# Kernel tuning notes

Measured on AMD Instinct MI355X. Metric: run time of the kernel, lower is better.

The kernel has to match this reference:

```python
import jax, jax.numpy as jnp
import numpy as np
from jax import lax

C = 256   # cnn_channels == rnn_in_dim
H = 256   # rnn_out_dim
NB = 16   # nb_classes
B, T, F = 16, 512, 40


def setup_inputs() -> dict:
    key = jax.random.key(0)
    ks = jax.random.split(key, 16)
    d = {
        'x': jax.random.normal(ks[0], (B, T, F), jnp.float32),
        'w1': jax.random.normal(ks[1], (C, 1, 5, 5), jnp.float32) * 0.05,
        'b1': jax.random.normal(ks[2], (C,), jnp.float32) * 0.05,
        'g1': jax.random.uniform(ks[3], (C,), jnp.float32, 0.5, 1.5),
        'bt1': jax.random.normal(ks[4], (C,), jnp.float32) * 0.05,
        'm1': jnp.zeros((C,), jnp.float32),
        'v1': jnp.ones((C,), jnp.float32),
        'w2': jax.random.normal(ks[5], (C, C, 5, 5), jnp.float32) * 0.02,
        'b2': jax.random.normal(ks[6], (C,), jnp.float32) * 0.05,
        'g2': jax.random.uniform(ks[7], (C,), jnp.float32, 0.5, 1.5),
        'bt2': jax.random.normal(ks[8], (C,), jnp.float32) * 0.05,
        'm2': jnp.zeros((C,), jnp.float32),
        'v2': jnp.ones((C,), jnp.float32),
        'w3': jax.random.normal(ks[9], (C, C, 5, 5), jnp.float32) * 0.02,
        'b3': jax.random.normal(ks[10], (C,), jnp.float32) * 0.05,
        'g3': jax.random.uniform(ks[11], (C,), jnp.float32, 0.5, 1.5),
        'bt3': jax.random.normal(ks[12], (C,), jnp.float32) * 0.05,
        'm3': jnp.zeros((C,), jnp.float32),
        'v3': jnp.ones((C,), jnp.float32),
        'w_ih': jax.random.normal(ks[13], (3 * H, C), jnp.float32) * 0.05,
        'w_hh': jax.random.normal(ks[14], (3 * H, H), jnp.float32) * 0.05,
        'b_ih': jnp.zeros((3 * H,), jnp.float32),
        'b_hh': jnp.zeros((3 * H,), jnp.float32),
        'w_cls': jax.random.normal(ks[15], (NB, H), jnp.float32) * 0.05,
        'b_cls': jnp.zeros((NB,), jnp.float32),
    }
    return d


def _conv_block(x, w, b, g, bt, m, v, pool):
    # Conv2d(k=5, pad=2) + BN (eval mode) + ReLU + MaxPool over freq axis
    y = lax.conv_general_dilated(x, w, (1, 1), ((2, 2), (2, 2)),
                                 dimension_numbers=('NCHW', 'OIHW', 'NCHW'))
    y = y + b[None, :, None, None]
    y = (y - m[None, :, None, None]) * (g * lax.rsqrt(v + 1e-5))[None, :, None, None] + bt[None, :, None, None]
    y = jnp.maximum(y, 0.0)
    y = lax.reduce_window(y, -jnp.inf, lax.max, (1, 1, 1, pool), (1, 1, 1, pool), 'VALID')
    return y


def _crnn(x, w1, b1, g1, bt1, m1, v1, w2, b2, g2, bt2, m2, v2,
          w3, b3, g3, bt3, m3, v3, w_ih, w_hh, b_ih, b_hh, w_cls, b_cls):
    b_size, t_steps, _ = x.shape
    y = x[:, None, :, :]                              # [B,1,T,F]
    y = _conv_block(y, w1, b1, g1, bt1, m1, v1, 5)    # [B,C,T,8]
    y = _conv_block(y, w2, b2, g2, bt2, m2, v2, 4)    # [B,C,T,2]
    y = _conv_block(y, w3, b3, g3, bt3, m3, v3, 2)    # [B,C,T,1]
    feats = jnp.transpose(y, (0, 2, 1, 3)).reshape(b_size, t_steps, C)  # [B,T,C]

    # Precompute input-side GRU gates for all steps (math identical to per-step)
    gi_all = jnp.einsum('btc,gc->btg', feats, w_ih) + b_ih  # [B,T,3H]

    def step(h, gi_t):
        gh = h @ w_hh.T + b_hh                        # [B,3H]
        r = jax.nn.sigmoid(gi_t[:, :H] + gh[:, :H])
        z = jax.nn.sigmoid(gi_t[:, H:2 * H] + gh[:, H:2 * H])
        n = jnp.tanh(gi_t[:, 2 * H:] + r * gh[:, 2 * H:])
        h_new = (1.0 - z) * n + z * h
        out = h_new @ w_cls.T + b_cls                 # [B,NB]
        return h_new, out

    h0 = jnp.zeros((b_size, H), feats.dtype)
    _, outs = lax.scan(step, h0, jnp.swapaxes(gi_all, 0, 1))  # [T,B,NB]
    return jnp.swapaxes(outs, 0, 1)                   # [B,T,NB]


def reference(x, w1, b1, g1, bt1, m1, v1, w2, b2, g2, bt2, m2, v2,
              w3, b3, g3, bt3, m3, v3, w_ih, w_hh, b_ih, b_hh, w_cls, b_cls):
    return _crnn(x, w1, b1, g1, bt1, m1, v1, w2, b2, g2, bt2, m2, v2,
                 w3, b3, g3, bt3, m3, v3, w_ih, w_hh, b_ih, b_hh, w_cls, b_cls)
```

## Files before the change

kernel.cpp:

```cpp
#include <hip/hip_runtime.h>
#include <hip/hip_bf16.h>
#include <math.h>

#define BB 16
#define TT 512
#define FF 40
#define CC 256
#define HH 256
#define GG 768
#define NB 16

typedef _Float16 f16;
typedef __attribute__((ext_vector_type(8))) _Float16 f16x8;
typedef __attribute__((ext_vector_type(4))) _Float16 f16x4;
typedef __attribute__((ext_vector_type(4))) float f32x4;

#define O_OUT1 0u
#define O_GI   0u
#define O_OUT2 16777216u
#define O_OUT3 20971520u
#define O_W2P  23068672u
#define O_W3P  24707072u
#define O_WIHP 26345472u
#define O_WHHP 26443776u

__device__ __forceinline__ float sigm_fast(float x) {
    return __builtin_amdgcn_rcpf(1.f + __expf(-x));
}
__device__ __forceinline__ float tanh_fast(float x) {
    return 1.f - 2.f * __builtin_amdgcn_rcpf(1.f + __expf(2.f * x));
}

__device__ __forceinline__ float sel4(f32x4 v, int q1, int q2) {
    float lo = q1 ? v[1] : v[0];
    float hi = q1 ? v[3] : v[2];
    return q2 ? hi : lo;
}

__device__ __forceinline__ void pack768(const float* __restrict__ src, f16* __restrict__ dst, int e) {
    int lane = e & 63;
    int r1 = e >> 6;
    int tile = r1 % 48, kf = r1 / 48;
    int g = tile * 16 + (lane & 15);
    int k0 = kf * 32 + (lane >> 4) * 8;
    f16x8 v;
#pragma unroll
    for (int j = 0; j < 8; ++j)
        v[j] = (f16)src[(size_t)g * HH + k0 + j];
    *(f16x8*)(dst + (size_t)e * 8) = v;
}

__global__ __launch_bounds__(256) void pack_all_kernel(
    const float* __restrict__ w2, const float* __restrict__ w3,
    const float* __restrict__ wih, const float* __restrict__ whh,
    const float* __restrict__ wcls,
    f16* __restrict__ w2p, f16* __restrict__ w3p, f16* __restrict__ wihp,
    f16* __restrict__ whhp, f16* __restrict__ wclsp) {
    int blk = blockIdx.x;
    int tid = threadIdx.x;
    if (blk < 800) {
        int e = blk * 256 + tid;
        int lane = e & 63;
        int r1 = e >> 6;
        int ntile = r1 & 15;
        int r2 = r1 >> 4;
        int cs4 = r2 & 3;
        int r3 = r2 >> 2;
        int cs = r3 & 1;
        int tap = r3 >> 1;
        int co = ntile * 16 + (lane & 15);
        int ci0 = cs * 128 + cs4 * 32 + (lane >> 4) * 8;
        f16x8 v;
#pragma unroll
        for (int j = 0; j < 8; ++j)
            v[j] = (f16)w2[(size_t)co * 6400 + (ci0 + j) * 25 + tap];
        *(f16x8*)(w2p + (size_t)e * 8) = v;
    } else if (blk < 1280) {
        int e = (blk - 800) * 256 + tid;
        int lane = e & 63;
        int r1 = e >> 6;
        int ntile = r1 & 15;
        int r2 = r1 >> 4;
        int cs4 = r2 & 3;
        int r3 = r2 >> 2;
        int cs = r3 & 1;
        int tap = r3 >> 1;
        int kh = tap / 3, kw = tap % 3 + 1;
        int co = ntile * 16 + (lane & 15);
        int ci0 = cs * 128 + cs4 * 32 + (lane >> 4) * 8;
        f16x8 v;
#pragma unroll
        for (int j = 0; j < 8; ++j)
            v[j] = (f16)w3[(size_t)co * 6400 + (ci0 + j) * 25 + kh * 5 + kw];
        *(f16x8*)(w3p + (size_t)e * 8) = v;
    } else if (blk < 1376) {
        pack768(wih, wihp, (blk - 1280) * 256 + tid);
    } else if (blk < 1472) {
        pack768(whh, whhp, (blk - 1376) * 256 + tid);
    } else {
#pragma unroll
        for (int i = 0; i < 2; ++i) {
            int e = tid + i * 256;
            int lane = e & 63, kf = e >> 6;
            int nb = lane & 15;
            int c0 = kf * 32 + (lane >> 4) * 8;
            f16x8 v;
#pragma unroll
            for (int j = 0; j < 8; ++j)
                v[j] = (f16)wcls[nb * HH + c0 + j];
            *(f16x8*)(wclsp + (size_t)e * 8) = v;
        }
    }
}

__global__ __launch_bounds__(256) void conv1_kernel(
    const float* __restrict__ x, const float* __restrict__ w1,
    const float* __restrict__ b1, const float* __restrict__ g1,
    const float* __restrict__ bt1, const float* __restrict__ m1,
    const float* __restrict__ v1, f16* __restrict__ out1h) {
    int h = blockIdx.x;
    int b = blockIdx.y;
    int c = threadIdx.x;
    __shared__ float xs[5][44];
    int t = threadIdx.x;
    if (t < 220) {
        int rr = t / 44, cc = t % 44;
        int hh = h + rr - 2, ww = cc - 2;
        float v = 0.f;
        if (hh >= 0 && hh < TT && ww >= 0 && ww < FF) v = x[(b * TT + hh) * FF + ww];
        xs[rr][cc] = v;
    }
    __syncthreads();
    float wr[25];
#pragma unroll
    for (int i = 0; i < 25; ++i) wr[i] = w1[c * 25 + i];
    float sc = g1[c] * rsqrtf(v1[c] + 1e-5f);
    float sh = (b1[c] - m1[c]) * sc + bt1[c];
    float conv[40];
#pragma unroll
    for (int w = 0; w < 40; ++w) conv[w] = 0.f;
#pragma unroll
    for (int kh = 0; kh < 5; ++kh) {
        float rr[44];
#pragma unroll
        for (int i = 0; i < 44; ++i) rr[i] = xs[kh][i];
#pragma unroll
        for (int kw = 0; kw < 5; ++kw) {
            float wv = wr[kh * 5 + kw];
#pragma unroll
            for (int w = 0; w < 40; ++w) conv[w] += rr[w + kw] * wv;
        }
    }
    f16* op = out1h + ((size_t)(b * TT + h) * 8) * CC + c;
#pragma unroll
    for (int j = 0; j < 8; ++j) {
        float m = 0.f;
#pragma unroll
        for (int p = 0; p < 5; ++p) m = fmaxf(m, conv[j * 5 + p] * sc + sh);
        op[j * CC] = (f16)m;
    }
}

__global__ __launch_bounds__(256) void conv2_mfma_kernel(
    const f16* __restrict__ in, const f16* __restrict__ w2p,
    const float* __restrict__ b2, const float* __restrict__ g2,
    const float* __restrict__ bt2, const float* __restrict__ m2,
    const float* __restrict__ v2, f16* __restrict__ out2h) {
    int htile = blockIdx.x;
    int b = blockIdx.y;
    int h0 = htile * 8;
    int t = threadIdx.x;
    int lane = t & 63, wid = t >> 6;
    int m16 = lane & 15, kq = lane >> 4;

    __shared__ f16 lds_a[12 * 12 * 136];

#pragma unroll
    for (int i = 0; i < 39; ++i) {
        int idx = t + i * 256;
        if (idx < 9792) ((unsigned*)lds_a)[idx] = 0u;
    }
    __syncthreads();

    f32x4 acc[4][4];
#pragma unroll
    for (int mf = 0; mf < 4; ++mf)
#pragma unroll
        for (int nf = 0; nf < 4; ++nf) acc[mf][nf] = (f32x4)(0.f);

    for (int cs = 0; cs < 2; ++cs) {
        if (cs) __syncthreads();
#pragma unroll
        for (int i = 0; i < 6; ++i) {
            int q = t + i * 256;
            int row = q >> 7, rem = q & 127;
            int w = rem >> 4, ci8 = (rem & 15) * 8;
            int hp = h0 - 2 + row;
            f16x8 v = (f16x8)((f16)0.f);
            if (hp >= 0 && hp < TT)
                v = *(const f16x8*)&in[((size_t)(b * TT + hp) * 8 + w) * CC + cs * 128 + ci8];
            *(f16x8*)&lds_a[row * 1632 + (w + 2) * 136 + ci8] = v;
        }
        __syncthreads();
        for (int kh = 0; kh < 5; ++kh) {
#pragma unroll
            for (int kw = 0; kw < 5; ++kw) {
                int tap = kh * 5 + kw;
#pragma unroll
                for (int cs4 = 0; cs4 < 4; ++cs4) {
                    f16x8 af[4];
#pragma unroll
                    for (int mf = 0; mf < 4; ++mf) {
                        int m = mf * 16 + m16;
                        int row = (m >> 3) + kh;
                        int wp = (m & 7) + kw;
                        af[mf] = *(const f16x8*)&lds_a[row * 1632 + wp * 136 + cs4 * 32 + kq * 8];
                    }
                    const f16x8* bp = (const f16x8*)w2p
                        + ((size_t)(((tap * 2 + cs) * 4 + cs4) * 16 + wid * 4) * 64 + lane);
#pragma unroll
                    for (int nf = 0; nf < 4; ++nf) {
                        f16x8 bf = bp[nf * 64];
#pragma unroll
                        for (int mf = 0; mf < 4; ++mf)
                            acc[mf][nf] = __builtin_amdgcn_mfma_f32_16x16x32_f16(af[mf], bf, acc[mf][nf], 0, 0, 0);
                    }
                }
            }
        }
    }

#pragma unroll
    for (int nf = 0; nf < 4; ++nf) {
        int co = wid * 64 + nf * 16 + m16;
        float sc = g2[co] * rsqrtf(v2[co] + 1e-5f);
        float sh = (b2[co] - m2[co]) * sc + bt2[co];
#pragma unroll
        for (int mf = 0; mf < 4; ++mf) {
            f32x4 v = acc[mf][nf];
            float p = 0.f;
            p = fmaxf(p, v[0] * sc + sh);
            p = fmaxf(p, v[1] * sc + sh);
            p = fmaxf(p, v[2] * sc + sh);
            p = fmaxf(p, v[3] * sc + sh);
            int dh = mf * 2 + (kq >> 1);
            int wout = kq & 1;
            out2h[((size_t)(b * TT + h0 + dh) * 2 + wout) * CC + co] = (f16)p;
        }
    }
}

__global__ __launch_bounds__(256) void conv3gi_kernel(
    const f16* __restrict__ in, const f16* __restrict__ w3p,
    const float* __restrict__ b3, const float* __restrict__ g3,
    const float* __restrict__ bt3, const float* __restrict__ m3,
    const float* __restrict__ v3, const f16* __restrict__ wihp,
    const float* __restrict__ bih, f16* __restrict__ gi2) {
    int htile = blockIdx.x;
    int b = blockIdx.y;
    int h0 = htile * 16;
    int t = threadIdx.x;
    int lane = t & 63, wid = t >> 6;
    int m16 = lane & 15, quad = lane >> 4;
    int rb = m16 >> 1, wv = m16 & 1;

    __shared__ f16 lds_a[20 * 6 * 136];
    __shared__ f16 feats_s[16 * 264];

    for (int i = t; i < 8160; i += 256) ((unsigned*)lds_a)[i] = 0u;
    __syncthreads();

    f32x4 acc[2][4];
#pragma unroll
    for (int mf = 0; mf < 2; ++mf)
#pragma unroll
        for (int nf = 0; nf < 4; ++nf) acc[mf][nf] = (f32x4)(0.f);

    for (int cs = 0; cs < 2; ++cs) {
        if (cs) __syncthreads();
#pragma unroll
        for (int i = 0; i < 3; ++i) {
            int q = t + i * 256;
            if (q < 640) {
                int row = q >> 5, rem = q & 31;
                int w = rem >> 4, ci8 = (rem & 15) * 8;
                int hp = h0 - 2 + row;
                f16x8 v = (f16x8)((f16)0.f);
                if (hp >= 0 && hp < TT)
                    v = *(const f16x8*)&in[((size_t)(b * TT + hp) * 2 + w) * CC + cs * 128 + ci8];
                *(f16x8*)&lds_a[row * 816 + (w + 2) * 136 + ci8] = v;
            }
        }
        __syncthreads();
        for (int kh = 0; kh < 5; ++kh) {
#pragma unroll
            for (int kw3 = 0; kw3 < 3; ++kw3) {
                int tap = kh * 3 + kw3;
#pragma unroll
                for (int cs4 = 0; cs4 < 4; ++cs4) {
                    f16x8 af[2];
#pragma unroll
                    for (int mf = 0; mf < 2; ++mf) {
                        int row = mf * 8 + rb + kh;
                        int wp = wv + kw3 + 1;
                        af[mf] = *(const f16x8*)&lds_a[row * 816 + wp * 136 + cs4 * 32 + quad * 8];
                    }
                    const f16x8* bp = (const f16x8*)w3p
                        + ((size_t)(((tap * 2 + cs) * 4 + cs4) * 16 + wid * 4) * 64 + lane);
#pragma unroll
                    for (int nf = 0; nf < 4; ++nf) {
                        f16x8 bf = bp[nf * 64];
#pragma unroll
                        for (int mf = 0; mf < 2; ++mf)
                            acc[mf][nf] = __builtin_amdgcn_mfma_f32_16x16x32_f16(af[mf], bf, acc[mf][nf], 0, 0, 0);
                    }
                }
            }
        }
    }

#pragma unroll
    for (int nf = 0; nf < 4; ++nf) {
        int co = wid * 64 + nf * 16 + m16;
        float sc = g3[co] * rsqrtf(v3[co] + 1e-5f);
        float sh = (b3[co] - m3[co]) * sc + bt3[co];
#pragma unroll
        for (int mf = 0; mf < 2; ++mf) {
            f32x4 v = acc[mf][nf];
            float p0 = fmaxf(0.f, fmaxf(v[0], v[1]) * sc + sh);
            p0 = fmaxf(p0, fmaxf(0.f, fminf(v[0], v[1]) * sc + sh));
            float p1 = fmaxf(0.f, fmaxf(v[2], v[3]) * sc + sh);
            p1 = fmaxf(p1, fmaxf(0.f, fminf(v[2], v[3]) * sc + sh));
            int m = mf * 8 + quad * 2;
            feats_s[m * 264 + co] = (f16)p0;
            feats_s[(m + 1) * 264 + co] = (f16)p1;
        }
    }
    __syncthreads();

    f32x4 gacc[12];
#pragma unroll
    for (int i = 0; i < 12; ++i) gacc[i] = (f32x4)(0.f);
#pragma unroll
    for (int kf = 0; kf < 8; ++kf) {
        f16x8 af = *(const f16x8*)&feats_s[m16 * 264 + kf * 32 + quad * 8];
#pragma unroll
        for (int nt = 0; nt < 12; ++nt) {
            f16x8 bf = ((const f16x8*)wihp)[(size_t)(kf * 48 + wid * 12 + nt) * 64 + lane];
            gacc[nt] = __builtin_amdgcn_mfma_f32_16x16x32_f16(af, bf, gacc[nt], 0, 0, 0);
        }
    }
#pragma unroll
    for (int nt = 0; nt < 12; ++nt) {
        int g = (wid * 12 + nt) * 16 + m16;
        float bv = bih[g];
#pragma unroll
        for (int r = 0; r < 4; ++r) {
            int s = h0 + quad * 4 + r;
            gi2[((((size_t)(b >> 2) * TT + s) * GG + g) << 2) + (b & 3)] = (f16)(gacc[nt][r] + bv);
        }
    }
}

__global__ __launch_bounds__(1024) void gru_mfma_kernel(
    const f16* __restrict__ gi2, const f16* __restrict__ whhp,
    const float* __restrict__ bhh, f16* __restrict__ hsave) {
    int blk = blockIdx.x;
    int t = threadIdx.x;
    int w = t >> 6, lane = t & 63;
    int n16 = lane & 15, quad = lane >> 4;
    int r2 = n16 & 3;
    int q1 = quad & 1, q2 = quad >> 1;
    __shared__ f16 hA[2][4 * 272];

    for (int i = t; i < 1088; i += 1024) ((unsigned*)hA)[i] = 0u;

    f16x8 wfrag[8][3];
#pragma unroll
    for (int kf = 0; kf < 8; ++kf)
#pragma unroll
        for (int g = 0; g < 3; ++g)
            wfrag[kf][g] = ((const f16x8*)whhp)[(size_t)(kf * 48 + g * 16 + w) * 64 + lane];
#pragma unroll
    for (int kf = 0; kf < 8; ++kf)
#pragma unroll
        for (int g = 0; g < 3; ++g)
            asm volatile("" : "+v"(wfrag[kf][g]));

    int c = w * 16 + n16;
    float bh0 = bhh[c], bh1 = bhh[HH + c], bh2 = bhh[2 * HH + c];
    float hold = 0.f;
    f16 hprev = (f16)0.f;
    int bg = blk * 4 + quad;

    const f16* gbase = gi2 + (size_t)blk * ((size_t)TT * GG * 4);
    int go0 = c * 4 + quad;
    int go1 = (c + HH) * 4 + quad;
    int go2 = (c + 2 * HH) * 4 + quad;

    f16 gc0 = gbase[go0];
    f16 gc1 = gbase[go1];
    f16 gc2 = gbase[go2];
    const f16* gp = gbase + GG * 4;
    __syncthreads();

    for (int s = 0; s < TT; ++s) {
        const f16* hrow = &hA[s & 1][r2 * 272 + quad * 8];
        f16x8 af[8];
#pragma unroll
        for (int kf = 0; kf < 8; ++kf)
            af[kf] = *(const f16x8*)(hrow + kf * 32);

        f16 gn0 = gp[go0];
        f16 gn1 = gp[go1];
        f16 gn2 = gp[go2];
        gp += GG * 4;
        if (s > 0)
            hsave[((size_t)(s - 1) * 16 + bg) * HH + c] = hprev;

        float x0 = (float)gc0 + bh0;
        float x1 = (float)gc1 + bh1;
        float x2 = (float)gc2;

        f32x4 acc[3];
#pragma unroll
        for (int g = 0; g < 3; ++g) acc[g] = (f32x4)(0.f);
#pragma unroll
        for (int kf = 0; kf < 8; ++kf) {
#pragma unroll
            for (int g = 0; g < 3; ++g)
                acc[g] = __builtin_amdgcn_mfma_f32_16x16x32_f16(af[kf], wfrag[kf][g], acc[g], 0, 0, 0);
        }

        float a0 = sel4(acc[0], q1, q2);
        float a1 = sel4(acc[1], q1, q2);
        float a2 = sel4(acc[2], q1, q2);

        float rr = sigm_fast(x0 + a0);
        float zz = sigm_fast(x1 + a1);
        float nn = tanh_fast(x2 + rr * (bh2 + a2));
        hold = nn + zz * (hold - nn);
        f16 hv = (f16)hold;
        hprev = hv;
        hA[(s + 1) & 1][quad * 272 + c] = hv;
        gc0 = gn0; gc1 = gn1; gc2 = gn2;
        asm volatile("s_waitcnt lgkmcnt(0)\n\ts_barrier" ::: "memory");
    }
    hsave[((size_t)(TT - 1) * 16 + bg) * HH + c] = hprev;
}

__global__ __launch_bounds__(256) void cls_kernel(
    const f16* __restrict__ hsave, const f16* __restrict__ wclsp,
    const float* __restrict__ bcls, float* __restrict__ out) {
    int s = blockIdx.x * 4 + (threadIdx.x >> 6);
    int lane = threadIdx.x & 63;
    int n16 = lane & 15, quad = lane >> 4;
    f32x4 ac = (f32x4)(0.f);
#pragma unroll
    for (int kf = 0; kf < 8; ++kf) {
        f16x8 af = *(const f16x8*)&hsave[((size_t)s * 16 + n16) * 256 + kf * 32 + quad * 8];
        f16x8 bf = ((const f16x8*)wclsp)[kf * 64 + lane];
        ac = __builtin_amdgcn_mfma_f32_16x16x32_f16(af, bf, ac, 0, 0, 0);
    }
    float bc = bcls[n16];
#pragma unroll
    for (int r = 0; r < 4; ++r)
        out[((size_t)(quad * 4 + r) * TT + s) * NB + n16] = ac[r] + bc;
}

extern "C" void kernel_launch(void* const* d_in, const int* in_sizes, int n_in,
                              void* d_out, int out_size, void* d_ws, size_t ws_size,
                              hipStream_t stream) {
    const float* x    = (const float*)d_in[0];
    const float* w1   = (const float*)d_in[1];
    const float* b1   = (const float*)d_in[2];
    const float* g1   = (const float*)d_in[3];
    const float* bt1  = (const float*)d_in[4];
    const float* m1   = (const float*)d_in[5];
    const float* v1   = (const float*)d_in[6];
    const float* w2   = (const float*)d_in[7];
    const float* b2   = (const float*)d_in[8];
    const float* g2   = (const float*)d_in[9];
    const float* bt2  = (const float*)d_in[10];
    const float* m2   = (const float*)d_in[11];
    const float* v2   = (const float*)d_in[12];
    const float* w3   = (const float*)d_in[13];
    const float* b3   = (const float*)d_in[14];
    const float* g3   = (const float*)d_in[15];
    const float* bt3  = (const float*)d_in[16];
    const float* m3   = (const float*)d_in[17];
    const float* v3   = (const float*)d_in[18];
    const float* wih  = (const float*)d_in[19];
    const float* whh  = (const float*)d_in[20];
    const float* bih  = (const float*)d_in[21];
    const float* bhh  = (const float*)d_in[22];
    const float* wcls = (const float*)d_in[23];
    const float* bcls = (const float*)d_in[24];

    float* ws    = (float*)d_ws;
    f16*   out1h = (f16*)(ws + O_OUT1);
    f16*   out2h = (f16*)(ws + O_OUT2);
    f16*   gi2   = (f16*)(ws + O_GI);
    f16*   w2p   = (f16*)(ws + O_W2P);
    f16*   w3p   = (f16*)(ws + O_W3P);
    f16*   wclsp = (f16*)(ws + O_W3P) + 983040;
    f16*   wihp  = (f16*)(ws + O_WIHP);
    f16*   whhp  = (f16*)(ws + O_WHHP);
    f16*   hsave = (f16*)(ws + O_OUT3);
    float* fout  = (float*)d_out;

    pack_all_kernel<<<1473, 256, 0, stream>>>(w2, w3, wih, whh, wcls,
                                              w2p, w3p, wihp, whhp, wclsp);

    conv1_kernel<<<dim3(512, 16), 256, 0, stream>>>(x, w1, b1, g1, bt1, m1, v1, out1h);
    conv2_mfma_kernel<<<dim3(64, 16), 256, 0, stream>>>(out1h, w2p, b2, g2, bt2, m2, v2, out2h);

    conv3gi_kernel<<<dim3(32, 16), 256, 0, stream>>>(out2h, w3p, b3, g3, bt3, m3, v3,
                                                     wihp, bih, gi2);

    gru_mfma_kernel<<<4, 1024, 0, stream>>>(gi2, whhp, bhh, hsave);

    cls_kernel<<<128, 256, 0, stream>>>(hsave, wclsp, bcls, fout);
}
```

Baseline: 1.171 ms.

## Fuse weight packing into conv1 launch and prefetch conv2 second channel half

Merges the weight-packing kernel into the conv1 kernel as extra blocks, removing one launch and letting the packing run alongside conv1. In conv2, the global loads for the second 128-channel half are issued into registers before the first half's MFMA loop, so their latency overlaps that compute, and they are then written to LDS. This raises register pressure in conv2 by six f16x8 values per thread, which may lower occupancy.

```diff
diff --git a/kernel.cpp b/kernel.cpp
--- a/kernel.cpp
+++ b/kernel.cpp
@@ -50,79 +50,82 @@
     *(f16x8*)(dst + (size_t)e * 8) = v;
 }
 
-__global__ __launch_bounds__(256) void pack_all_kernel(
+__global__ __launch_bounds__(256) void conv1_pack_kernel(
+    const float* __restrict__ x, const float* __restrict__ w1,
+    const float* __restrict__ b1, const float* __restrict__ g1,
+    const float* __restrict__ bt1, const float* __restrict__ m1,
+    const float* __restrict__ v1, f16* __restrict__ out1h,
     const float* __restrict__ w2, const float* __restrict__ w3,
     const float* __restrict__ wih, const float* __restrict__ whh,
     const float* __restrict__ wcls,
     f16* __restrict__ w2p, f16* __restrict__ w3p, f16* __restrict__ wihp,
     f16* __restrict__ whhp, f16* __restrict__ wclsp) {
-    int blk = blockIdx.x;
+    __shared__ float xs[5][44];
+    int bid = blockIdx.x;
     int tid = threadIdx.x;
-    if (blk < 800) {
-        int e = blk * 256 + tid;
-        int lane = e & 63;
-        int r1 = e >> 6;
-        int ntile = r1 & 15;
-        int r2 = r1 >> 4;
-        int cs4 = r2 & 3;
-        int r3 = r2 >> 2;
-        int cs = r3 & 1;
-        int tap = r3 >> 1;
-        int co = ntile * 16 + (lane & 15);
-        int ci0 = cs * 128 + cs4 * 32 + (lane >> 4) * 8;
-        f16x8 v;
-#pragma unroll
-        for (int j = 0; j < 8; ++j)
-            v[j] = (f16)w2[(size_t)co * 6400 + (ci0 + j) * 25 + tap];
-        *(f16x8*)(w2p + (size_t)e * 8) = v;
-    } else if (blk < 1280) {
-        int e = (blk - 800) * 256 + tid;
-        int lane = e & 63;
-        int r1 = e >> 6;
-        int ntile = r1 & 15;
-        int r2 = r1 >> 4;
-        int cs4 = r2 & 3;
-        int r3 = r2 >> 2;
-        int cs = r3 & 1;
-        int tap = r3 >> 1;
-        int kh = tap / 3, kw = tap % 3 + 1;
-        int co = ntile * 16 + (lane & 15);
-        int ci0 = cs * 128 + cs4 * 32 + (lane >> 4) * 8;
-        f16x8 v;
-#pragma unroll
-        for (int j = 0; j < 8; ++j)
-            v[j] = (f16)w3[(size_t)co * 6400 + (ci0 + j) * 25 + kh * 5 + kw];
-        *(f16x8*)(w3p + (size_t)e * 8) = v;
-    } else if (blk < 1376) {
-        pack768(wih, wihp, (blk - 1280) * 256 + tid);
-    } else if (blk < 1472) {
-        pack768(whh, whhp, (blk - 1376) * 256 + tid);
-    } else {
-#pragma unroll
-        for (int i = 0; i < 2; ++i) {
-            int e = tid + i * 256;
-            int lane = e & 63, kf = e >> 6;
-            int nb = lane & 15;
-            int c0 = kf * 32 + (lane >> 4) * 8;
+
+    if (bid >= 8192) {
+        int blk = bid - 8192;
+        if (blk < 800) {
+            int e = blk * 256 + tid;
+            int lane = e & 63;
+            int r1 = e >> 6;
+            int ntile = r1 & 15;
+            int r2 = r1 >> 4;
+            int cs4 = r2 & 3;
+            int r3 = r2 >> 2;
+            int cs = r3 & 1;
+            int tap = r3 >> 1;
+            int co = ntile * 16 + (lane & 15);
+            int ci0 = cs * 128 + cs4 * 32 + (lane >> 4) * 8;
             f16x8 v;
 #pragma unroll
             for (int j = 0; j < 8; ++j)
-                v[j] = (f16)wcls[nb * HH + c0 + j];
-            *(f16x8*)(wclsp + (size_t)e * 8) = v;
-        }
-    }
-}
-
-__global__ __launch_bounds__(256) void conv1_kernel(
-    const float* __restrict__ x, const float* __restrict__ w1,
-    const float* __restrict__ b1, const float* __restrict__ g1,
-    const float* __restrict__ bt1, const float* __restrict__ m1,
-    const float* __restrict__ v1, f16* __restrict__ out1h) {
-    int h = blockIdx.x;
-    int b = blockIdx.y;
-    int c = threadIdx.x;
-    __shared__ float xs[5][44];
-    int t = threadIdx.x;
+                v[j] = (f16)w2[(size_t)co * 6400 + (ci0 + j) * 25 + tap];
+            *(f16x8*)(w2p + (size_t)e * 8) = v;
+        } else if (blk < 1280) {
+            int e = (blk - 800) * 256 + tid;
+            int lane = e & 63;
+            int r1 = e >> 6;
+            int ntile = r1 & 15;
+            int r2 = r1 >> 4;
+            int cs4 = r2 & 3;
+            int r3 = r2 >> 2;
+            int cs = r3 & 1;
+            int tap = r3 >> 1;
+            int kh = tap / 3, kw = tap % 3 + 1;
+            int co = ntile * 16 + (lane & 15);
+            int ci0 = cs * 128 + cs4 * 32 + (lane >> 4) * 8;
+            f16x8 v;
+#pragma unroll
+            for (int j = 0; j < 8; ++j)
+                v[j] = (f16)w3[(size_t)co * 6400 + (ci0 + j) * 25 + kh * 5 + kw];
+            *(f16x8*)(w3p + (size_t)e * 8) = v;
+        } else if (blk < 1376) {
+            pack768(wih, wihp, (blk - 1280) * 256 + tid);
+        } else if (blk < 1472) {
+            pack768(whh, whhp, (blk - 1376) * 256 + tid);
+        } else {
+#pragma unroll
+            for (int i = 0; i < 2; ++i) {
+                int e = tid + i * 256;
+                int lane = e & 63, kf = e >> 6;
+                int nb = lane & 15;
+                int c0 = kf * 32 + (lane >> 4) * 8;
+                f16x8 v;
+#pragma unroll
+                for (int j = 0; j < 8; ++j)
+                    v[j] = (f16)wcls[nb * HH + c0 + j];
+                *(f16x8*)(wclsp + (size_t)e * 8) = v;
+            }
+        }
+        return;
+    }
+
+    int b = bid >> 9;
+    int h = bid & 511;
+    int c = tid;
+    int t = tid;
     if (t < 220) {
         int rr = t / 44, cc = t % 44;
         int hh = h + rr - 2, ww = cc - 2;
@@ -188,47 +191,72 @@
 #pragma unroll
         for (int nf = 0; nf < 4; ++nf) acc[mf][nf] = (f32x4)(0.f);
 
-    for (int cs = 0; cs < 2; ++cs) {
-        if (cs) __syncthreads();
-#pragma unroll
-        for (int i = 0; i < 6; ++i) {
-            int q = t + i * 256;
-            int row = q >> 7, rem = q & 127;
-            int w = rem >> 4, ci8 = (rem & 15) * 8;
-            int hp = h0 - 2 + row;
-            f16x8 v = (f16x8)((f16)0.f);
-            if (hp >= 0 && hp < TT)
-                v = *(const f16x8*)&in[((size_t)(b * TT + hp) * 8 + w) * CC + cs * 128 + ci8];
-            *(f16x8*)&lds_a[row * 1632 + (w + 2) * 136 + ci8] = v;
-        }
-        __syncthreads();
-        for (int kh = 0; kh < 5; ++kh) {
-#pragma unroll
-            for (int kw = 0; kw < 5; ++kw) {
-                int tap = kh * 5 + kw;
-#pragma unroll
-                for (int cs4 = 0; cs4 < 4; ++cs4) {
-                    f16x8 af[4];
-#pragma unroll
-                    for (int mf = 0; mf < 4; ++mf) {
-                        int m = mf * 16 + m16;
-                        int row = (m >> 3) + kh;
-                        int wp = (m & 7) + kw;
-                        af[mf] = *(const f16x8*)&lds_a[row * 1632 + wp * 136 + cs4 * 32 + kq * 8];
-                    }
-                    const f16x8* bp = (const f16x8*)w2p
-                        + ((size_t)(((tap * 2 + cs) * 4 + cs4) * 16 + wid * 4) * 64 + lane);
-#pragma unroll
-                    for (int nf = 0; nf < 4; ++nf) {
-                        f16x8 bf = bp[nf * 64];
-#pragma unroll
-                        for (int mf = 0; mf < 4; ++mf)
-                            acc[mf][nf] = __builtin_amdgcn_mfma_f32_16x16x32_f16(af[mf], bf, acc[mf][nf], 0, 0, 0);
-                    }
-                }
-            }
-        }
-    }
+#pragma unroll
+    for (int i = 0; i < 6; ++i) {
+        int q = t + i * 256;
+        int row = q >> 7, rem = q & 127;
+        int w = rem >> 4, ci8 = (rem & 15) * 8;
+        int hp = h0 - 2 + row;
+        f16x8 v = (f16x8)((f16)0.f);
+        if (hp >= 0 && hp < TT)
+            v = *(const f16x8*)&in[((size_t)(b * TT + hp) * 8 + w) * CC + ci8];
+        *(f16x8*)&lds_a[row * 1632 + (w + 2) * 136 + ci8] = v;
+    }
+    __syncthreads();
+
+    f16x8 pre[6];
+#pragma unroll
+    for (int i = 0; i < 6; ++i) {
+        int q = t + i * 256;
+        int row = q >> 7, rem = q & 127;
+        int w = rem >> 4, ci8 = (rem & 15) * 8;
+        int hp = h0 - 2 + row;
+        pre[i] = (f16x8)((f16)0.f);
+        if (hp >= 0 && hp < TT)
+            pre[i] = *(const f16x8*)&in[((size_t)(b * TT + hp) * 8 + w) * CC + 128 + ci8];
+    }
+
+#define CONV2_MFMA_PHASE(CS)                                                                        \
+    for (int kh = 0; kh < 5; ++kh) {                                                                \
+        _Pragma("unroll")                                                                           \
+        for (int kw = 0; kw < 5; ++kw) {                                                            \
+            int tap = kh * 5 + kw;                                                                  \
+            _Pragma("unroll")                                                                       \
+            for (int cs4 = 0; cs4 < 4; ++cs4) {                                                     \
+                f16x8 af[4];                                                                        \
+                _Pragma("unroll")                                                                   \
+                for (int mf = 0; mf < 4; ++mf) {                                                    \
+                    int m = mf * 16 + m16;                                                          \
+                    int row = (m >> 3) + kh;                                                        \
+                    int wp = (m & 7) + kw;                                                          \
+                    af[mf] = *(const f16x8*)&lds_a[row * 1632 + wp * 136 + cs4 * 32 + kq * 8];      \
+                }                                                                                   \
+                const f16x8* bp = (const f16x8*)w2p                                                 \
+                    + ((size_t)(((tap * 2 + (CS)) * 4 + cs4) * 16 + wid * 4) * 64 + lane);          \
+                _Pragma("unroll")                                                                   \
+                for (int nf = 0; nf < 4; ++nf) {                                                    \
+                    f16x8 bf = bp[nf * 64];                                                         \
+                    _Pragma("unroll")                                                               \
+                    for (int mf = 0; mf < 4; ++mf)                                                  \
+                        acc[mf][nf] = __builtin_amdgcn_mfma_f32_16x16x32_f16(af[mf], bf,            \
+                                                                             acc[mf][nf], 0, 0, 0); \
+                }                                                                                   \
+            }                                                                                       \
+        }                                                                                           \
+    }
+
+    CONV2_MFMA_PHASE(0)
+    __syncthreads();
+#pragma unroll
+    for (int i = 0; i < 6; ++i) {
+        int q = t + i * 256;
+        int row = q >> 7, rem = q & 127;
+        int w = rem >> 4, ci8 = (rem & 15) * 8;
+        *(f16x8*)&lds_a[row * 1632 + (w + 2) * 136 + ci8] = pre[i];
+    }
+    __syncthreads();
+    CONV2_MFMA_PHASE(1)
+#undef CONV2_MFMA_PHASE
 
 #pragma unroll
     for (int nf = 0; nf < 4; ++nf) {
@@ -509,10 +537,10 @@
     f16*   hsave = (f16*)(ws + O_OUT3);
     float* fout  = (float*)d_out;
 
-    pack_all_kernel<<<1473, 256, 0, stream>>>(w2, w3, wih, whh, wcls,
-                                              w2p, w3p, wihp, whhp, wclsp);
-
-    conv1_kernel<<<dim3(512, 16), 256, 0, stream>>>(x, w1, b1, g1, bt1, m1, v1, out1h);
+    conv1_pack_kernel<<<9665, 256, 0, stream>>>(x, w1, b1, g1, bt1, m1, v1, out1h,
+                                                w2, w3, wih, whh, wcls,
+                                                w2p, w3p, wihp, whhp, wclsp);
+
     conv2_mfma_kernel<<<dim3(64, 16), 256, 0, stream>>>(out1h, w2p, b2, g2, bt2, m2, v2, out2h);
 
     conv3gi_kernel<<<dim3(32, 16), 256, 0, stream>>>(out2h, w3p, b3, g3, bt3, m3, v3,
```

Measured after the change: 1.162 ms (median of 2 runs). No clear change (-0.7%).
